# Kernel optimization log

Hardware: AMD Instinct MI355X
Metric: run time of the kernel (lower is better)

Reference implementation:

```python
import jax, jax.numpy as jnp
import numpy as np

B, H, W, DIM, WS, NH, HID = 16, 64, 64, 256, 8, 8, 1024
SHIFT = WS // 2
N = WS * WS  # tokens per window


def _rel_pos_index(ws):
    coords = np.stack(np.meshgrid(np.arange(ws), np.arange(ws), indexing='ij')).reshape(2, -1)
    rel = (coords[:, :, None] - coords[:, None, :]).transpose(1, 2, 0)  # [n,n,2]
    rel[..., 0] += ws - 1
    rel[..., 1] += ws - 1
    rel[..., 0] *= 2 * ws - 1
    return rel.sum(-1)  # [n,n] ints in [0, (2ws-1)^2)


def _attn_mask(h, w, ws, ss):
    img = np.zeros((h, w), np.float32)
    cnt = 0
    sl = (slice(0, -ws), slice(-ws, -ss), slice(-ss, None))
    for hs in sl:
        for wsl in sl:
            img[hs, wsl] = cnt
            cnt += 1
    mw = img.reshape(h // ws, ws, w // ws, ws).transpose(0, 2, 1, 3).reshape(-1, ws * ws)
    d = mw[:, None, :] - mw[:, :, None]  # unsqueeze(1) - unsqueeze(2)
    return np.where(d != 0, np.float32(-100.0), np.float32(0.0))  # [nW,n,n]


RPI = jnp.asarray(_rel_pos_index(WS).reshape(-1))          # [n*n] int
MASK = jnp.asarray(_attn_mask(H, W, WS, SHIFT))            # [nW,n,n]


def ln(x, g, b, eps):
    m = x.mean(-1, keepdims=True)
    v = x.var(-1, keepdims=True)
    return (x - m) / jnp.sqrt(v + eps) * g + b


def win_part(x, ws):
    b, h, w, c = x.shape
    x = x.reshape(b, h // ws, ws, w // ws, ws, c).transpose(0, 1, 3, 2, 4, 5)
    return x.reshape(-1, ws * ws, c)  # [b*nW, n, c]


def win_rev(win, ws, h, w):
    c = win.shape[-1]
    b = win.shape[0] // ((h // ws) * (w // ws))
    x = win.reshape(b, h // ws, w // ws, ws, ws, c).transpose(0, 1, 3, 2, 4, 5)
    return x.reshape(b, h, w, c)


def attention(xw, qkv_w, qkv_b, rpb, out_w, out_b, mask):
    Bw, n, c = xw.shape
    dh = c // NH
    scale = dh ** -0.5
    qkv = (xw @ qkv_w + qkv_b).reshape(Bw, n, 3, NH, dh).transpose(2, 0, 3, 1, 4)
    q, k, v = qkv[0], qkv[1], qkv[2]                       # [Bw,NH,n,dh]
    dots = jnp.einsum('bhid,bhjd->bhij', q, k) * scale
    bias = rpb[RPI].reshape(n, n, NH).transpose(2, 0, 1)   # [NH,n,n]
    attn = dots + bias[None]
    if mask is not None:
        nW = mask.shape[0]
        attn = attn.reshape(Bw // nW, nW, NH, n, n) + mask[None, :, None]
        attn = attn.reshape(Bw, NH, n, n)
    attn = jax.nn.softmax(attn, axis=-1)
    out = jnp.einsum('bhij,bhjd->bhid', attn, v)
    out = out.transpose(0, 2, 1, 3).reshape(Bw, n, c)
    return out @ out_w + out_b


def block(x, shifted, mask, n1g, n1b, qkv_w, qkv_b, rpb, out_w, out_b,
          n2g, n2b, lng, lnb, w1, b1, w2, b2):
    b, l, c = x.shape
    shortcut = x
    x = ln(x, n1g, n1b, 1e-5).reshape(b, H, W, c)
    if shifted:
        x = jnp.roll(x, (-SHIFT, -SHIFT), (1, 2))
    xw = win_part(x, WS)
    xw = attention(xw, qkv_w, qkv_b, rpb, out_w, out_b, mask)
    x = win_rev(xw, WS, H, W)
    if shifted:
        x = jnp.roll(x, (SHIFT, SHIFT), (1, 2))
    x = shortcut + x.reshape(b, l, c)
    # FeedForward contains its own LayerNorm(eps=1e-6) after norm2 (faithful to source)
    h = ln(x, n2g, n2b, 1e-5)
    h = ln(h, lng, lnb, 1e-6)
    h = jax.nn.gelu(h @ w1 + b1, approximate=False) @ w2 + b2
    return x + h


def forward(x, *p):
    x = block(x, False, None, *p[0:15])
    x = block(x, True, MASK, *p[15:30])
    return x


def setup_inputs() -> dict:
    key = jax.random.key(0)
    ks = iter(jax.random.split(key, 16))
    s = 0.02
    d = {'x': jax.random.normal(next(ks), (B, H * W, DIM), jnp.float32)}
    for i in (0, 1):
        p = f'b{i}_'
        d[p + 'n1g'] = jnp.ones((DIM,), jnp.float32)
        d[p + 'n1b'] = jnp.zeros((DIM,), jnp.float32)
        d[p + 'qkv_w'] = jax.random.normal(next(ks), (DIM, 3 * DIM), jnp.float32) * s
        d[p + 'qkv_b'] = jnp.zeros((3 * DIM,), jnp.float32)
        d[p + 'rpb'] = jax.random.normal(next(ks), ((2 * WS - 1) ** 2, NH), jnp.float32) * s
        d[p + 'out_w'] = jax.random.normal(next(ks), (DIM, DIM), jnp.float32) * s
        d[p + 'out_b'] = jnp.zeros((DIM,), jnp.float32)
        d[p + 'n2g'] = jnp.ones((DIM,), jnp.float32)
        d[p + 'n2b'] = jnp.zeros((DIM,), jnp.float32)
        d[p + 'lng'] = jnp.ones((DIM,), jnp.float32)
        d[p + 'lnb'] = jnp.zeros((DIM,), jnp.float32)
        d[p + 'w1'] = jax.random.normal(next(ks), (DIM, HID), jnp.float32) * s
        d[p + 'b1'] = jnp.zeros((HID,), jnp.float32)
        d[p + 'w2'] = jax.random.normal(next(ks), (HID, DIM), jnp.float32) * s
        d[p + 'b2'] = jnp.zeros((DIM,), jnp.float32)
    return d


def reference(x,
              b0_n1g, b0_n1b, b0_qkv_w, b0_qkv_b, b0_rpb, b0_out_w, b0_out_b,
              b0_n2g, b0_n2b, b0_lng, b0_lnb, b0_w1, b0_b1, b0_w2, b0_b2,
              b1_n1g, b1_n1b, b1_qkv_w, b1_qkv_b, b1_rpb, b1_out_w, b1_out_b,
              b1_n2g, b1_n2b, b1_lng, b1_lnb, b1_w1, b1_b1, b1_w2, b1_b2):
    return forward(x,
                   b0_n1g, b0_n1b, b0_qkv_w, b0_qkv_b, b0_rpb, b0_out_w, b0_out_b,
                   b0_n2g, b0_n2b, b0_lng, b0_lnb, b0_w1, b0_b1, b0_w2, b0_b2,
                   b1_n1g, b1_n1b, b1_qkv_w, b1_qkv_b, b1_rpb, b1_out_w, b1_out_b,
                   b1_n2g, b1_n2b, b1_lng, b1_lnb, b1_w1, b1_b1, b1_w2, b1_b2)
```

## Files before the change

### kernel.cpp

```cpp
#include <hip/hip_runtime.h>

typedef unsigned short u16;
typedef __attribute__((ext_vector_type(8))) short bf16x8;
typedef __attribute__((ext_vector_type(8))) unsigned short u16x8;
typedef __attribute__((ext_vector_type(4))) unsigned short u16x4;
typedef __attribute__((ext_vector_type(4))) float f32x4;

__device__ inline float b2f(u16 u) {
    union { unsigned u32; float f; } x; x.u32 = ((unsigned)u) << 16; return x.f;
}
__device__ inline u16 f2b(float f) {
    union { float f; unsigned u; } x; x.f = f;
    unsigned r = x.u + 0x7fffu + ((x.u >> 16) & 1u);
    return (u16)(r >> 16);
}

#define GLOAD_LDS16(g, l) \
    __builtin_amdgcn_global_load_lds((const __attribute__((address_space(1))) void*)(const void*)(g), \
                                     (__attribute__((address_space(3))) void*)(void*)(l), 16, 0, 0)

__global__ __launch_bounds__(256)
void ln_win_kernel(const float* __restrict__ x, const float* __restrict__ g,
                   const float* __restrict__ b, u16* __restrict__ xw, int shift)
{
    int wid = blockIdx.x * 4 + (threadIdx.x >> 6);
    int lane = threadIdx.x & 63;
    int win = wid >> 6, tok = wid & 63;
    int bb = win >> 6, wib = win & 63;
    int h = (((wib >> 3) << 3) + (tok >> 3) + shift) & 63;
    int w = (((wib & 7) << 3) + (tok & 7) + shift) & 63;
    size_t src = ((size_t)bb * 4096 + h * 64 + w) * 256;
    float4 v = ((const float4*)(x + src))[lane];
    float s = v.x + v.y + v.z + v.w;
    float s2 = v.x*v.x + v.y*v.y + v.z*v.z + v.w*v.w;
    for (int k = 32; k > 0; k >>= 1) { s += __shfl_xor(s, k); s2 += __shfl_xor(s2, k); }
    float mean = s * (1.f/256.f);
    float var  = s2 * (1.f/256.f) - mean*mean;
    float rs = rsqrtf(var + 1e-5f);
    int c = lane * 4;
    u16x4 o;
    o[0] = f2b((v.x - mean) * rs * g[c+0] + b[c+0]);
    o[1] = f2b((v.y - mean) * rs * g[c+1] + b[c+1]);
    o[2] = f2b((v.z - mean) * rs * g[c+2] + b[c+2]);
    o[3] = f2b((v.w - mean) * rs * g[c+3] + b[c+3]);
    *(u16x4*)(xw + (size_t)wid * 256 + c) = o;
}

__global__ __launch_bounds__(256)
void ln2_kernel(const float* __restrict__ xin,
                const float* __restrict__ g1, const float* __restrict__ b1,
                const float* __restrict__ g2, const float* __restrict__ b2,
                u16* __restrict__ out)
{
    int wid = blockIdx.x * 4 + (threadIdx.x >> 6);
    int lane = threadIdx.x & 63;
    float4 v = ((const float4*)(xin + (size_t)wid * 256))[lane];
    float s = v.x + v.y + v.z + v.w;
    float s2 = v.x*v.x + v.y*v.y + v.z*v.z + v.w*v.w;
    for (int k = 32; k > 0; k >>= 1) { s += __shfl_xor(s, k); s2 += __shfl_xor(s2, k); }
    float mean = s * (1.f/256.f);
    float var  = s2 * (1.f/256.f) - mean*mean;
    float rs = rsqrtf(var + 1e-5f);
    int c = lane * 4;
    float y0 = (v.x - mean) * rs * g1[c+0] + b1[c+0];
    float y1 = (v.y - mean) * rs * g1[c+1] + b1[c+1];
    float y2 = (v.z - mean) * rs * g1[c+2] + b1[c+2];
    float y3 = (v.w - mean) * rs * g1[c+3] + b1[c+3];
    float t = y0 + y1 + y2 + y3;
    float t2 = y0*y0 + y1*y1 + y2*y2 + y3*y3;
    for (int k = 32; k > 0; k >>= 1) { t += __shfl_xor(t, k); t2 += __shfl_xor(t2, k); }
    float m2 = t * (1.f/256.f);
    float v2 = t2 * (1.f/256.f) - m2*m2;
    float rs2 = rsqrtf(v2 + 1e-6f);
    u16x4 o;
    o[0] = f2b((y0 - m2) * rs2 * g2[c+0] + b2[c+0]);
    o[1] = f2b((y1 - m2) * rs2 * g2[c+1] + b2[c+1]);
    o[2] = f2b((y2 - m2) * rs2 * g2[c+2] + b2[c+2]);
    o[3] = f2b((y3 - m2) * rs2 * g2[c+3] + b2[c+3]);
    *(u16x4*)(out + (size_t)wid * 256 + c) = o;
}

__global__ __launch_bounds__(256)
void transpose_w(const float* __restrict__ W, u16* __restrict__ Wt, int K, int N)
{
    __shared__ float t[32][33];
    int nb = blockIdx.x * 32, kb = blockIdx.y * 32;
    int tx = threadIdx.x & 31, ty = threadIdx.x >> 5;
    #pragma unroll
    for (int r = 0; r < 32; r += 8)
        t[ty + r][tx] = W[(size_t)(kb + ty + r) * N + nb + tx];
    __syncthreads();
    #pragma unroll
    for (int r = 0; r < 32; r += 8)
        Wt[(size_t)(nb + ty + r) * K + kb + tx] = f2b(t[tx][ty + r]);
}

__global__ __launch_bounds__(256)
void build_bias(const float* __restrict__ rpb, float* __restrict__ bmT)
{
    int idx = blockIdx.x * 256 + threadIdx.x;
    int q = idx & 63, k = (idx >> 6) & 63, h = (idx >> 12) & 7, cls = idx >> 15;
    int qh = q >> 3, qw = q & 7, kh = k >> 3, kw = k & 7;
    float v = rpb[((qh - kh + 7) * 15 + (qw - kw + 7)) * 8 + h];
    int ch = cls >> 1, cw = cls & 1;
    int rq = (ch ? (qh < 4 ? 1 : 2) : 0) * 3 + (cw ? (qw < 4 ? 1 : 2) : 0);
    int rk = (ch ? (kh < 4 ? 1 : 2) : 0) * 3 + (cw ? (kw < 4 ? 1 : 2) : 0);
    if (rq != rk) v -= 100.f;
    bmT[idx] = v * 1.4426950408889634f;
}

template<int EPI>
__global__ __launch_bounds__(256)
void gemm_bf16(const u16* __restrict__ A, const u16* __restrict__ Bt,
               const float* __restrict__ bias, void* __restrict__ out,
               const float* __restrict__ resid, int M, int N, int K, int shift)
{
    __shared__ u16 As[128 * 32];
    __shared__ u16 Bs[128 * 32];
    const int tid = threadIdx.x;
    const int lane = tid & 63, wv = tid >> 6;
    const int bm = blockIdx.y, bn = blockIdx.x;
    const int wr = wv >> 1, wc = wv & 1;
    f32x4 acc[4][4] = {};
    const int arow = wv * 16 + (lane >> 2);
    const int acol = (lane & 3) * 8;
    const u16* gA = A + (size_t)(bm * 128 + arow) * K + acol;
    const u16* gB = Bt + (size_t)(bn * 128 + arow) * K + acol;
    const int nk = K >> 5;
    for (int kt = 0; kt < nk; ++kt) {
        __syncthreads();
        GLOAD_LDS16(gA,          As + wv * 512);
        GLOAD_LDS16(gA + 64 * K, As + 2048 + wv * 512);
        GLOAD_LDS16(gB,          Bs + wv * 512);
        GLOAD_LDS16(gB + 64 * K, Bs + 2048 + wv * 512);
        gA += 32; gB += 32;
        __syncthreads();
        const int g = lane >> 4, r = lane & 15;
        bf16x8 af[4], bf[4];
        #pragma unroll
        for (int i = 0; i < 4; ++i)
            af[i] = *(const bf16x8*)(As + (wr * 64 + i * 16 + r) * 32 + g * 8);
        #pragma unroll
        for (int i = 0; i < 4; ++i)
            bf[i] = *(const bf16x8*)(Bs + (wc * 64 + i * 16 + r) * 32 + g * 8);
        #pragma unroll
        for (int i = 0; i < 4; ++i)
            #pragma unroll
            for (int j = 0; j < 4; ++j)
                acc[i][j] = __builtin_amdgcn_mfma_f32_16x16x32_bf16(af[i], bf[j], acc[i][j], 0, 0, 0);
    }
    const int r4 = (lane >> 4) * 4;
    const int cn = lane & 15;
    #pragma unroll
    for (int i = 0; i < 4; ++i) {
        #pragma unroll
        for (int rr = 0; rr < 4; ++rr) {
            int row = bm * 128 + wr * 64 + i * 16 + r4 + rr;
            size_t orow;
            if (EPI == 2) {
                int win = row >> 6, tok = row & 63;
                int bb = win >> 6, wib = win & 63;
                int h = (((wib >> 3) << 3) + (tok >> 3) + shift) & 63;
                int w = (((wib & 7) << 3) + (tok & 7) + shift) & 63;
                orow = (size_t)bb * 4096 + h * 64 + w;
            } else {
                orow = (size_t)row;
            }
            #pragma unroll
            for (int j = 0; j < 4; ++j) {
                int col = bn * 128 + wc * 64 + j * 16 + cn;
                float v = acc[i][j][rr] + bias[col];
                if (EPI == 0) {
                    ((u16*)out)[(size_t)row * N + col] = f2b(v);
                } else if (EPI == 1) {
                    float ge = 0.5f * v * (1.f + erff(v * 0.70710678118654752f));
                    ((u16*)out)[(size_t)row * N + col] = f2b(ge);
                } else {
                    ((float*)out)[orow * N + col] = resid[orow * N + col] + v;
                }
            }
        }
    }
}

template<int SHIFTED>
__global__ __launch_bounds__(256)
void attn_mfma(const u16* __restrict__ qkv, const float* __restrict__ bmT,
               u16* __restrict__ out)
{
    __shared__ u16 pbuf[4][64 * 72];
    __shared__ u16 vbuf[4][32 * 72];
    const int tid = threadIdx.x, lane = tid & 63, wv = tid >> 6;
    const int g = lane >> 4, r = lane & 15;
    const int win = blockIdx.x;
    u16* P  = pbuf[wv];
    u16* Vt = vbuf[wv];
    const u16* base = qkv + (size_t)win * 64 * 768;
    int cls = 0;
    if (SHIFTED) {
        int wib = win & 63;
        cls = (((wib >> 3) == 7) ? 2 : 0) + (((wib & 7) == 7) ? 1 : 0);
    }
    const float sc = 0.17677669529663687f * 1.4426950408889634f;

    for (int hh = 0; hh < 2; ++hh) {
        const int h = wv * 2 + hh;
        const float* bmh = bmT + ((size_t)cls * 8 + h) * 4096;
        bf16x8 kf[4], qf[4];
        #pragma unroll
        for (int i = 0; i < 4; ++i) {
            kf[i] = *(const bf16x8*)(base + (size_t)(i * 16 + r) * 768 + 256 + h * 32 + g * 8);
            qf[i] = *(const bf16x8*)(base + (size_t)(i * 16 + r) * 768 +       h * 32 + g * 8);
        }
        #pragma unroll
        for (int d0 = 0; d0 < 32; d0 += 8) {
            u16x8 vv = *(const u16x8*)(base + (size_t)lane * 768 + 512 + h * 32 + d0);
            #pragma unroll
            for (int e = 0; e < 8; ++e) Vt[(d0 + e) * 72 + lane] = vv[e];
        }
        f32x4 acc[4][4] = {};
        #pragma unroll
        for (int i = 0; i < 4; ++i)
            #pragma unroll
            for (int j = 0; j < 4; ++j)
                acc[i][j] = __builtin_amdgcn_mfma_f32_16x16x32_bf16(kf[i], qf[j], acc[i][j], 0, 0, 0);
        #pragma unroll
        for (int i = 0; i < 4; ++i) {
            const int kb = (i * 16 + g * 4) * 64;
            #pragma unroll
            for (int j = 0; j < 4; ++j) {
                const int qq = j * 16 + r;
                #pragma unroll
                for (int rr = 0; rr < 4; ++rr)
                    acc[i][j][rr] = acc[i][j][rr] * sc + bmh[kb + rr * 64 + qq];
            }
        }
        float inv_[4];
        #pragma unroll
        for (int j = 0; j < 4; ++j) {
            float m = acc[0][j][0];
            #pragma unroll
            for (int i = 0; i < 4; ++i)
                #pragma unroll
                for (int rr = 0; rr < 4; ++rr) m = fmaxf(m, acc[i][j][rr]);
            m = fmaxf(m, __shfl_xor(m, 16));
            m = fmaxf(m, __shfl_xor(m, 32));
            float s = 0.f;
            #pragma unroll
            for (int i = 0; i < 4; ++i)
                #pragma unroll
                for (int rr = 0; rr < 4; ++rr) {
                    float p = exp2f(acc[i][j][rr] - m);
                    acc[i][j][rr] = p; s += p;
                }
            s += __shfl_xor(s, 16);
            s += __shfl_xor(s, 32);
            inv_[j] = 1.f / s;
        }
        #pragma unroll
        for (int j = 0; j < 4; ++j) {
            const float iv = inv_[j];
            #pragma unroll
            for (int i = 0; i < 4; ++i) {
                u16x4 w;
                #pragma unroll
                for (int rr = 0; rr < 4; ++rr) w[rr] = f2b(acc[i][j][rr] * iv);
                *(u16x4*)(P + (j * 16 + r) * 72 + i * 16 + g * 4) = w;
            }
        }
        f32x4 o[4][2] = {};
        #pragma unroll
        for (int ks = 0; ks < 2; ++ks) {
            bf16x8 pa[4], vb[2];
            #pragma unroll
            for (int i = 0; i < 4; ++i)
                pa[i] = *(const bf16x8*)(P + (i * 16 + r) * 72 + ks * 32 + g * 8);
            #pragma unroll
            for (int j = 0; j < 2; ++j)
                vb[j] = *(const bf16x8*)(Vt + (j * 16 + r) * 72 + ks * 32 + g * 8);
            #pragma unroll
            for (int i = 0; i < 4; ++i)
                #pragma unroll
                for (int j = 0; j < 2; ++j)
                    o[i][j] = __builtin_amdgcn_mfma_f32_16x16x32_bf16(pa[i], vb[j], o[i][j], 0, 0, 0);
        }
        u16* op = out + (size_t)win * 64 * 256 + h * 32;
        #pragma unroll
        for (int i = 0; i < 4; ++i)
            #pragma unroll
            for (int j = 0; j < 2; ++j)
                #pragma unroll
                for (int rr = 0; rr < 4; ++rr)
                    op[(size_t)(i * 16 + g * 4 + rr) * 256 + j * 16 + r] = f2b(o[i][j][rr]);
    }
}

extern "C" void kernel_launch(void* const* d_in, const int* in_sizes, int n_in,
                              void* d_out, int out_size, void* d_ws, size_t ws_size,
                              hipStream_t stream)
{
    (void)in_sizes; (void)n_in; (void)out_size; (void)ws_size;
    const float* x = (const float*)d_in[0];
    char* ws = (char*)d_ws;
    size_t off = 0;
    auto alloc = [&](size_t bytes) { void* p = ws + off; off += (bytes + 255) & ~(size_t)255; return p; };

    u16 *wtq[2], *wto[2], *wt1[2], *wt2[2];
    float* bmT[2];
    for (int i = 0; i < 2; ++i) {
        wtq[i] = (u16*)alloc((size_t)768 * 256 * 2);
        wto[i] = (u16*)alloc((size_t)256 * 256 * 2);
        wt1[i] = (u16*)alloc((size_t)1024 * 256 * 2);
        wt2[i] = (u16*)alloc((size_t)256 * 1024 * 2);
        bmT[i] = (float*)alloc((size_t)4 * 8 * 64 * 64 * 4);
    }
    u16*  xw  = (u16*)alloc((size_t)65536 * 256 * 2);
    u16*  big = (u16*)alloc((size_t)65536 * 1024 * 2);
    float* x1 = (float*)alloc((size_t)65536 * 256 * 4);
    float* outp = (float*)d_out;

    for (int blk = 0; blk < 2; ++blk) {
        const float* const* P = (const float* const*)(d_in + 1 + blk * 15);
        transpose_w<<<dim3(768 / 32, 256 / 32), 256, 0, stream>>>(P[2], wtq[blk], 256, 768);
        transpose_w<<<dim3(256 / 32, 256 / 32), 256, 0, stream>>>(P[5], wto[blk], 256, 256);
        transpose_w<<<dim3(1024 / 32, 256 / 32), 256, 0, stream>>>(P[11], wt1[blk], 256, 1024);
        transpose_w<<<dim3(256 / 32, 1024 / 32), 256, 0, stream>>>(P[13], wt2[blk], 1024, 256);
        build_bias<<<512, 256, 0, stream>>>(P[4], bmT[blk]);
    }

    for (int blk = 0; blk < 2; ++blk) {
        const float* const* P = (const float* const*)(d_in + 1 + blk * 15);
        const int sh = blk ? 4 : 0;
        const float* xin = blk ? outp : x;

        ln_win_kernel<<<16384, 256, 0, stream>>>(xin, P[0], P[1], xw, sh);
        gemm_bf16<0><<<dim3(6, 512), 256, 0, stream>>>(xw, wtq[blk], P[3], big, nullptr, 65536, 768, 256, 0);
        if (blk) attn_mfma<1><<<1024, 256, 0, stream>>>(big, bmT[blk], xw);
        else     attn_mfma<0><<<1024, 256, 0, stream>>>(big, bmT[blk], xw);
        gemm_bf16<2><<<dim3(2, 512), 256, 0, stream>>>(xw, wto[blk], P[6], x1, xin, 65536, 256, 256, sh);
        ln2_kernel<<<16384, 256, 0, stream>>>(x1, P[7], P[8], P[9], P[10], xw);
        gemm_bf16<1><<<dim3(8, 512), 256, 0, stream>>>(xw, wt1[blk], P[12], big, nullptr, 65536, 1024, 256, 0);
        gemm_bf16<3><<<dim3(2, 512), 256, 0, stream>>>(big, wt2[blk], P[14], outp, x1, 65536, 256, 1024, 0);
    }
}
```

Measured before the change: 748.8 us.

## Fuse MLP GEMMs with GELU through LDS and vectorize GEMM epilogues

Replaces the separate fc1+GELU and fc2+residual GEMMs with one fused kernel that keeps the 1024-wide hidden activations for a 64-row tile in shared memory, avoiding writing and re-reading the large hidden tensor. GEMM and attention MFMA operands are swapped so each lane holds contiguous columns, enabling vectorized bias/residual loads and stores. The GEMM grid is remapped so consecutive tiles land on the same XCD. The fused kernel loads operands straight from global memory without LDS staging, relying on caches for weight reuse.

```diff
diff --git a/kernel.cpp b/kernel.cpp
--- a/kernel.cpp
+++ b/kernel.cpp
@@ -119,7 +119,12 @@
     __shared__ u16 Bs[128 * 32];
     const int tid = threadIdx.x;
     const int lane = tid & 63, wv = tid >> 6;
-    const int bm = blockIdx.y, bn = blockIdx.x;
+    const int nwg = gridDim.x * gridDim.y;
+    const int lid = blockIdx.y * gridDim.x + blockIdx.x;
+    const int qq = nwg >> 3, r8 = nwg & 7;
+    const int xcd = lid & 7, pos = lid >> 3;
+    const int nid = (xcd < r8 ? xcd * (qq + 1) : r8 * (qq + 1) + (xcd - r8) * qq) + pos;
+    const int bm = nid / gridDim.x, bn = nid % gridDim.x;
     const int wr = wv >> 1, wc = wv & 1;
     f32x4 acc[4][4] = {};
     const int arow = wv * 16 + (lane >> 2);
@@ -127,6 +132,7 @@
     const u16* gA = A + (size_t)(bm * 128 + arow) * K + acol;
     const u16* gB = Bt + (size_t)(bn * 128 + arow) * K + acol;
     const int nk = K >> 5;
+    const int g = lane >> 4, r = lane & 15;
     for (int kt = 0; kt < nk; ++kt) {
         __syncthreads();
         GLOAD_LDS16(gA,          As + wv * 512);
@@ -135,7 +141,6 @@
         GLOAD_LDS16(gB + 64 * K, Bs + 2048 + wv * 512);
         gA += 32; gB += 32;
         __syncthreads();
-        const int g = lane >> 4, r = lane & 15;
         bf16x8 af[4], bf[4];
         #pragma unroll
         for (int i = 0; i < 4; ++i)
@@ -144,41 +149,125 @@
         for (int i = 0; i < 4; ++i)
             bf[i] = *(const bf16x8*)(Bs + (wc * 64 + i * 16 + r) * 32 + g * 8);
         #pragma unroll
-        for (int i = 0; i < 4; ++i)
-            #pragma unroll
-            for (int j = 0; j < 4; ++j)
-                acc[i][j] = __builtin_amdgcn_mfma_f32_16x16x32_bf16(af[i], bf[j], acc[i][j], 0, 0, 0);
-    }
-    const int r4 = (lane >> 4) * 4;
-    const int cn = lane & 15;
+        for (int j = 0; j < 4; ++j)
+            #pragma unroll
+            for (int i = 0; i < 4; ++i)
+                acc[j][i] = __builtin_amdgcn_mfma_f32_16x16x32_bf16(bf[j], af[i], acc[j][i], 0, 0, 0);
+    }
     #pragma unroll
     for (int i = 0; i < 4; ++i) {
-        #pragma unroll
-        for (int rr = 0; rr < 4; ++rr) {
-            int row = bm * 128 + wr * 64 + i * 16 + r4 + rr;
-            size_t orow;
-            if (EPI == 2) {
-                int win = row >> 6, tok = row & 63;
-                int bb = win >> 6, wib = win & 63;
-                int h = (((wib >> 3) << 3) + (tok >> 3) + shift) & 63;
-                int w = (((wib & 7) << 3) + (tok & 7) + shift) & 63;
-                orow = (size_t)bb * 4096 + h * 64 + w;
+        const int row = bm * 128 + wr * 64 + i * 16 + r;
+        size_t orow;
+        if (EPI == 2) {
+            int win = row >> 6, tok = row & 63;
+            int bb = win >> 6, wib = win & 63;
+            int h = (((wib >> 3) << 3) + (tok >> 3) + shift) & 63;
+            int w = (((wib & 7) << 3) + (tok & 7) + shift) & 63;
+            orow = (size_t)bb * 4096 + h * 64 + w;
+        } else {
+            orow = (size_t)row;
+        }
+        #pragma unroll
+        for (int j = 0; j < 4; ++j) {
+            const int colb = bn * 128 + wc * 64 + j * 16 + g * 4;
+            const float4 bv = *(const float4*)(bias + colb);
+            if (EPI == 0) {
+                u16x4 o;
+                o[0] = f2b(acc[j][i][0] + bv.x);
+                o[1] = f2b(acc[j][i][1] + bv.y);
+                o[2] = f2b(acc[j][i][2] + bv.z);
+                o[3] = f2b(acc[j][i][3] + bv.w);
+                *(u16x4*)((u16*)out + (size_t)row * N + colb) = o;
             } else {
-                orow = (size_t)row;
+                const float4 rv = *(const float4*)(resid + orow * N + colb);
+                float4 o;
+                o.x = rv.x + acc[j][i][0] + bv.x;
+                o.y = rv.y + acc[j][i][1] + bv.y;
+                o.z = rv.z + acc[j][i][2] + bv.z;
+                o.w = rv.w + acc[j][i][3] + bv.w;
+                *(float4*)((float*)out + orow * N + colb) = o;
             }
-            #pragma unroll
-            for (int j = 0; j < 4; ++j) {
-                int col = bn * 128 + wc * 64 + j * 16 + cn;
-                float v = acc[i][j][rr] + bias[col];
-                if (EPI == 0) {
-                    ((u16*)out)[(size_t)row * N + col] = f2b(v);
-                } else if (EPI == 1) {
-                    float ge = 0.5f * v * (1.f + erff(v * 0.70710678118654752f));
-                    ((u16*)out)[(size_t)row * N + col] = f2b(ge);
-                } else {
-                    ((float*)out)[orow * N + col] = resid[orow * N + col] + v;
+        }
+    }
+}
+
+__global__ __launch_bounds__(256, 2)
+void fused_mlp(const u16* __restrict__ A, const u16* __restrict__ W1t,
+               const float* __restrict__ b1, const u16* __restrict__ W2t,
+               const float* __restrict__ b2, const float* __restrict__ x1,
+               float* __restrict__ out)
+{
+    __shared__ u16 Hs[64][264];
+    const int tid = threadIdx.x, lane = tid & 63, wv = tid >> 6;
+    const int g = lane >> 4, r = lane & 15;
+    const size_t row0 = (size_t)blockIdx.x * 64;
+    f32x4 p2[4][4] = {};
+    for (int q = 0; q < 4; ++q) {
+        f32x4 p1[4][4] = {};
+        const u16* w1p = W1t + ((size_t)q * 256 + wv * 64) * 256;
+        #pragma unroll
+        for (int ks = 0; ks < 8; ++ks) {
+            bf16x8 af[4], wb[4];
+            #pragma unroll
+            for (int i = 0; i < 4; ++i)
+                af[i] = *(const bf16x8*)(A + (row0 + i * 16 + r) * 256 + ks * 32 + g * 8);
+            #pragma unroll
+            for (int j = 0; j < 4; ++j)
+                wb[j] = *(const bf16x8*)(w1p + (size_t)(j * 16 + r) * 256 + ks * 32 + g * 8);
+            #pragma unroll
+            for (int j = 0; j < 4; ++j)
+                #pragma unroll
+                for (int i = 0; i < 4; ++i)
+                    p1[j][i] = __builtin_amdgcn_mfma_f32_16x16x32_bf16(wb[j], af[i], p1[j][i], 0, 0, 0);
+        }
+        __syncthreads();
+        #pragma unroll
+        for (int j = 0; j < 4; ++j) {
+            const int cq = wv * 64 + j * 16 + g * 4;
+            const float4 bv = *(const float4*)(b1 + q * 256 + cq);
+            #pragma unroll
+            for (int i = 0; i < 4; ++i) {
+                u16x4 hw;
+                #pragma unroll
+                for (int rr = 0; rr < 4; ++rr) {
+                    float v = p1[j][i][rr] + ((const float*)&bv)[rr];
+                    hw[rr] = f2b(0.5f * v * (1.f + erff(v * 0.70710678118654752f)));
                 }
+                *(u16x4*)(&Hs[i * 16 + r][cq]) = hw;
             }
+        }
+        __syncthreads();
+        const u16* w2p = W2t + (size_t)(wv * 64) * 1024 + q * 256;
+        #pragma unroll
+        for (int ks = 0; ks < 8; ++ks) {
+            bf16x8 hf[4], w2[4];
+            #pragma unroll
+            for (int i = 0; i < 4; ++i)
+                hf[i] = *(const bf16x8*)(&Hs[i * 16 + r][ks * 32 + g * 8]);
+            #pragma unroll
+            for (int j = 0; j < 4; ++j)
+                w2[j] = *(const bf16x8*)(w2p + (size_t)(j * 16 + r) * 1024 + ks * 32 + g * 8);
+            #pragma unroll
+            for (int j = 0; j < 4; ++j)
+                #pragma unroll
+                for (int i = 0; i < 4; ++i)
+                    p2[j][i] = __builtin_amdgcn_mfma_f32_16x16x32_bf16(w2[j], hf[i], p2[j][i], 0, 0, 0);
+        }
+    }
+    #pragma unroll
+    for (int j = 0; j < 4; ++j) {
+        const int col = wv * 64 + j * 16 + g * 4;
+        const float4 bv = *(const float4*)(b2 + col);
+        #pragma unroll
+        for (int i = 0; i < 4; ++i) {
+            const size_t row = row0 + i * 16 + r;
+            const float4 rv = *(const float4*)(x1 + row * 256 + col);
+            float4 o;
+            o.x = rv.x + p2[j][i][0] + bv.x;
+            o.y = rv.y + p2[j][i][1] + bv.y;
+            o.z = rv.z + p2[j][i][2] + bv.z;
+            o.w = rv.w + p2[j][i][3] + bv.w;
+            *(float4*)(out + row * 256 + col) = o;
         }
     }
 }
@@ -268,7 +357,7 @@
                 *(u16x4*)(P + (j * 16 + r) * 72 + i * 16 + g * 4) = w;
             }
         }
-        f32x4 o[4][2] = {};
+        f32x4 o[2][4] = {};
         #pragma unroll
         for (int ks = 0; ks < 2; ++ks) {
             bf16x8 pa[4], vb[2];
@@ -279,19 +368,23 @@
             for (int j = 0; j < 2; ++j)
                 vb[j] = *(const bf16x8*)(Vt + (j * 16 + r) * 72 + ks * 32 + g * 8);
             #pragma unroll
-            for (int i = 0; i < 4; ++i)
-                #pragma unroll
-                for (int j = 0; j < 2; ++j)
-                    o[i][j] = __builtin_amdgcn_mfma_f32_16x16x32_bf16(pa[i], vb[j], o[i][j], 0, 0, 0);
+            for (int j = 0; j < 2; ++j)
+                #pragma unroll
+                for (int i = 0; i < 4; ++i)
+                    o[j][i] = __builtin_amdgcn_mfma_f32_16x16x32_bf16(vb[j], pa[i], o[j][i], 0, 0, 0);
         }
         u16* op = out + (size_t)win * 64 * 256 + h * 32;
         #pragma unroll
-        for (int i = 0; i < 4; ++i)
-            #pragma unroll
-            for (int j = 0; j < 2; ++j)
-                #pragma unroll
-                for (int rr = 0; rr < 4; ++rr)
-                    op[(size_t)(i * 16 + g * 4 + rr) * 256 + j * 16 + r] = f2b(o[i][j][rr]);
+        for (int i = 0; i < 4; ++i) {
+            const int qrow = i * 16 + r;
+            #pragma unroll
+            for (int j = 0; j < 2; ++j) {
+                u16x4 w;
+                #pragma unroll
+                for (int rr = 0; rr < 4; ++rr) w[rr] = f2b(o[j][i][rr]);
+                *(u16x4*)(op + (size_t)qrow * 256 + j * 16 + g * 4) = w;
+            }
+        }
     }
 }
 
@@ -315,7 +408,7 @@
         bmT[i] = (float*)alloc((size_t)4 * 8 * 64 * 64 * 4);
     }
     u16*  xw  = (u16*)alloc((size_t)65536 * 256 * 2);
-    u16*  big = (u16*)alloc((size_t)65536 * 1024 * 2);
+    u16*  big = (u16*)alloc((size_t)65536 * 768 * 2);
     float* x1 = (float*)alloc((size_t)65536 * 256 * 4);
     float* outp = (float*)d_out;
 
@@ -339,7 +432,6 @@
         else     attn_mfma<0><<<1024, 256, 0, stream>>>(big, bmT[blk], xw);
         gemm_bf16<2><<<dim3(2, 512), 256, 0, stream>>>(xw, wto[blk], P[6], x1, xin, 65536, 256, 256, sh);
         ln2_kernel<<<16384, 256, 0, stream>>>(x1, P[7], P[8], P[9], P[10], xw);
-        gemm_bf16<1><<<dim3(8, 512), 256, 0, stream>>>(xw, wt1[blk], P[12], big, nullptr, 65536, 1024, 256, 0);
-        gemm_bf16<3><<<dim3(2, 512), 256, 0, stream>>>(big, wt2[blk], P[14], outp, x1, 65536, 256, 1024, 0);
-    }
-}
+        fused_mlp<<<1024, 256, 0, stream>>>(xw, wt1[blk], P[12], wt2[blk], P[14], x1, outp);
+    }
+}
```

Result: slower. 919.1 us (+22.7%).

## Pipeline GEMM with 4-stage LDS ring, swizzle, XCD remap, vectorized epilogues

Applied to the files above, without the earlier changes.

Replaces the single-buffered GEMM with a 4-slot LDS ring that prefetches two k-tiles ahead, using explicit vmcnt waits and one barrier per iteration. It XOR-swizzles LDS columns to avoid bank conflicts and remaps workgroups to XCDs for cache locality. Operands are swapped in the MFMA so each lane holds four consecutive columns, which allows vectorized bias, residual and output stores; the attention PV output uses the same trick. GELU switches to a polynomial erf approximation, which adds small numeric error.

```diff
diff --git a/kernel.cpp b/kernel.cpp
--- a/kernel.cpp
+++ b/kernel.cpp
@@ -15,9 +15,21 @@
     return (u16)(r >> 16);
 }
 
+__device__ inline float fast_gelu(float v) {
+    float x = fabsf(v) * 0.70710678118654752f;
+    float t = __builtin_amdgcn_rcpf(1.0f + 0.3275911f * x);
+    float e = __expf(-x * x);
+    float poly = ((((1.061405429f * t - 1.453152027f) * t + 1.421413741f) * t
+                   - 0.284496736f) * t + 0.254829592f) * t;
+    float erfv = 1.0f - poly * e;
+    float w = copysignf(erfv, v);
+    return 0.5f * v * (1.0f + w);
+}
+
 #define GLOAD_LDS16(g, l) \
     __builtin_amdgcn_global_load_lds((const __attribute__((address_space(1))) void*)(const void*)(g), \
                                      (__attribute__((address_space(3))) void*)(void*)(l), 16, 0, 0)
+#define FENCE() asm volatile("" ::: "memory")
 
 __global__ __launch_bounds__(256)
 void ln_win_kernel(const float* __restrict__ x, const float* __restrict__ g,
@@ -111,73 +123,110 @@
 
 template<int EPI>
 __global__ __launch_bounds__(256)
-void gemm_bf16(const u16* __restrict__ A, const u16* __restrict__ Bt,
-               const float* __restrict__ bias, void* __restrict__ out,
-               const float* __restrict__ resid, int M, int N, int K, int shift)
-{
-    __shared__ u16 As[128 * 32];
-    __shared__ u16 Bs[128 * 32];
-    const int tid = threadIdx.x;
-    const int lane = tid & 63, wv = tid >> 6;
-    const int bm = blockIdx.y, bn = blockIdx.x;
+void gemm_k4(const u16* __restrict__ A, const u16* __restrict__ Bt,
+             const float* __restrict__ bias, void* __restrict__ out,
+             const float* __restrict__ resid, int M, int N, int K, int shift)
+{
+    __shared__ u16 As[4][128][32];
+    __shared__ u16 Bs[4][128][32];
+    const int tid = threadIdx.x, lane = tid & 63, wv = tid >> 6;
+    const int g = lane >> 4, r = lane & 15;
     const int wr = wv >> 1, wc = wv & 1;
+    const int nwg = gridDim.x * gridDim.y;
+    const int lid = blockIdx.y * gridDim.x + blockIdx.x;
+    const int qq = nwg >> 3, r8 = nwg & 7;
+    const int xcd = lid & 7, pos = lid >> 3;
+    const int nid = (xcd < r8 ? xcd * (qq + 1) : r8 * (qq + 1) + (xcd - r8) * qq) + pos;
+    const int bm = nid / gridDim.x, bn = nid % gridDim.x;
+
     f32x4 acc[4][4] = {};
     const int arow = wv * 16 + (lane >> 2);
-    const int acol = (lane & 3) * 8;
-    const u16* gA = A + (size_t)(bm * 128 + arow) * K + acol;
-    const u16* gB = Bt + (size_t)(bn * 128 + arow) * K + acol;
+    const int scol = (((lane & 3) ^ ((lane >> 2) & 3) ^ ((lane >> 4) & 1)) * 8);
+    const u16* gA = A + (size_t)(bm * 128 + arow) * K + scol;
+    const u16* gB = Bt + (size_t)(bn * 128 + arow) * K + scol;
     const int nk = K >> 5;
+    const int rc = (g ^ (r & 3) ^ ((r >> 2) & 1)) * 8;
+
+#define STAGE(t) do { \
+        u16* a_ = &As[(t) & 3][0][0]; u16* b_ = &Bs[(t) & 3][0][0]; \
+        GLOAD_LDS16(gA + (size_t)(t) * 32,                    a_ + wv * 512); \
+        GLOAD_LDS16(gA + (size_t)(t) * 32 + (size_t)64 * K,   a_ + 2048 + wv * 512); \
+        GLOAD_LDS16(gB + (size_t)(t) * 32,                    b_ + wv * 512); \
+        GLOAD_LDS16(gB + (size_t)(t) * 32 + (size_t)64 * K,   b_ + 2048 + wv * 512); \
+    } while (0)
+
+    STAGE(0);
+    STAGE(1);
     for (int kt = 0; kt < nk; ++kt) {
-        __syncthreads();
-        GLOAD_LDS16(gA,          As + wv * 512);
-        GLOAD_LDS16(gA + 64 * K, As + 2048 + wv * 512);
-        GLOAD_LDS16(gB,          Bs + wv * 512);
-        GLOAD_LDS16(gB + 64 * K, Bs + 2048 + wv * 512);
-        gA += 32; gB += 32;
-        __syncthreads();
-        const int g = lane >> 4, r = lane & 15;
+        const int cur = kt & 3;
+        if (kt + 2 < nk) {
+            STAGE(kt + 2);
+            asm volatile("s_waitcnt vmcnt(8)" ::: "memory");
+        } else if (kt + 1 < nk) {
+            asm volatile("s_waitcnt vmcnt(4)" ::: "memory");
+        } else {
+            asm volatile("s_waitcnt vmcnt(0)" ::: "memory");
+        }
+        __builtin_amdgcn_s_barrier();
+        FENCE();
         bf16x8 af[4], bf[4];
         #pragma unroll
         for (int i = 0; i < 4; ++i)
-            af[i] = *(const bf16x8*)(As + (wr * 64 + i * 16 + r) * 32 + g * 8);
-        #pragma unroll
-        for (int i = 0; i < 4; ++i)
-            bf[i] = *(const bf16x8*)(Bs + (wc * 64 + i * 16 + r) * 32 + g * 8);
-        #pragma unroll
-        for (int i = 0; i < 4; ++i)
-            #pragma unroll
-            for (int j = 0; j < 4; ++j)
-                acc[i][j] = __builtin_amdgcn_mfma_f32_16x16x32_bf16(af[i], bf[j], acc[i][j], 0, 0, 0);
-    }
-    const int r4 = (lane >> 4) * 4;
-    const int cn = lane & 15;
+            af[i] = *(const bf16x8*)(&As[cur][wr * 64 + i * 16 + r][rc]);
+        #pragma unroll
+        for (int j = 0; j < 4; ++j)
+            bf[j] = *(const bf16x8*)(&Bs[cur][wc * 64 + j * 16 + r][rc]);
+        __builtin_amdgcn_s_setprio(1);
+        #pragma unroll
+        for (int j = 0; j < 4; ++j)
+            #pragma unroll
+            for (int i = 0; i < 4; ++i)
+                acc[j][i] = __builtin_amdgcn_mfma_f32_16x16x32_bf16(bf[j], af[i], acc[j][i], 0, 0, 0);
+        __builtin_amdgcn_s_setprio(0);
+        asm volatile("s_waitcnt lgkmcnt(0)" ::: "memory");
+        __builtin_amdgcn_sched_barrier(0);
+    }
+#undef STAGE
+
     #pragma unroll
     for (int i = 0; i < 4; ++i) {
-        #pragma unroll
-        for (int rr = 0; rr < 4; ++rr) {
-            int row = bm * 128 + wr * 64 + i * 16 + r4 + rr;
-            size_t orow;
-            if (EPI == 2) {
-                int win = row >> 6, tok = row & 63;
-                int bb = win >> 6, wib = win & 63;
-                int h = (((wib >> 3) << 3) + (tok >> 3) + shift) & 63;
-                int w = (((wib & 7) << 3) + (tok & 7) + shift) & 63;
-                orow = (size_t)bb * 4096 + h * 64 + w;
+        const int row = bm * 128 + wr * 64 + i * 16 + r;
+        size_t orow;
+        if (EPI == 2) {
+            int win = row >> 6, tok = row & 63;
+            int bb = win >> 6, wib = win & 63;
+            int h = (((wib >> 3) << 3) + (tok >> 3) + shift) & 63;
+            int w = (((wib & 7) << 3) + (tok & 7) + shift) & 63;
+            orow = (size_t)bb * 4096 + h * 64 + w;
+        } else {
+            orow = (size_t)row;
+        }
+        #pragma unroll
+        for (int j = 0; j < 4; ++j) {
+            const int colb = bn * 128 + wc * 64 + j * 16 + g * 4;
+            const float4 bv = *(const float4*)(bias + colb);
+            if (EPI == 0) {
+                u16x4 o;
+                o[0] = f2b(acc[j][i][0] + bv.x);
+                o[1] = f2b(acc[j][i][1] + bv.y);
+                o[2] = f2b(acc[j][i][2] + bv.z);
+                o[3] = f2b(acc[j][i][3] + bv.w);
+                *(u16x4*)((u16*)out + (size_t)row * N + colb) = o;
+            } else if (EPI == 1) {
+                u16x4 o;
+                o[0] = f2b(fast_gelu(acc[j][i][0] + bv.x));
+                o[1] = f2b(fast_gelu(acc[j][i][1] + bv.y));
+                o[2] = f2b(fast_gelu(acc[j][i][2] + bv.z));
+                o[3] = f2b(fast_gelu(acc[j][i][3] + bv.w));
+                *(u16x4*)((u16*)out + (size_t)row * N + colb) = o;
             } else {
-                orow = (size_t)row;
-            }
-            #pragma unroll
-            for (int j = 0; j < 4; ++j) {
-                int col = bn * 128 + wc * 64 + j * 16 + cn;
-                float v = acc[i][j][rr] + bias[col];
-                if (EPI == 0) {
-                    ((u16*)out)[(size_t)row * N + col] = f2b(v);
-                } else if (EPI == 1) {
-                    float ge = 0.5f * v * (1.f + erff(v * 0.70710678118654752f));
-                    ((u16*)out)[(size_t)row * N + col] = f2b(ge);
-                } else {
-                    ((float*)out)[orow * N + col] = resid[orow * N + col] + v;
-                }
+                const float4 rv = *(const float4*)(resid + orow * N + colb);
+                float4 o;
+                o.x = rv.x + acc[j][i][0] + bv.x;
+                o.y = rv.y + acc[j][i][1] + bv.y;
+                o.z = rv.z + acc[j][i][2] + bv.z;
+                o.w = rv.w + acc[j][i][3] + bv.w;
+                *(float4*)((float*)out + orow * N + colb) = o;
             }
         }
     }
@@ -268,7 +317,7 @@
                 *(u16x4*)(P + (j * 16 + r) * 72 + i * 16 + g * 4) = w;
             }
         }
-        f32x4 o[4][2] = {};
+        f32x4 o[2][4] = {};
         #pragma unroll
         for (int ks = 0; ks < 2; ++ks) {
             bf16x8 pa[4], vb[2];
@@ -279,19 +328,23 @@
             for (int j = 0; j < 2; ++j)
                 vb[j] = *(const bf16x8*)(Vt + (j * 16 + r) * 72 + ks * 32 + g * 8);
             #pragma unroll
-            for (int i = 0; i < 4; ++i)
-                #pragma unroll
-                for (int j = 0; j < 2; ++j)
-                    o[i][j] = __builtin_amdgcn_mfma_f32_16x16x32_bf16(pa[i], vb[j], o[i][j], 0, 0, 0);
+            for (int j = 0; j < 2; ++j)
+                #pragma unroll
+                for (int i = 0; i < 4; ++i)
+                    o[j][i] = __builtin_amdgcn_mfma_f32_16x16x32_bf16(vb[j], pa[i], o[j][i], 0, 0, 0);
         }
         u16* op = out + (size_t)win * 64 * 256 + h * 32;
         #pragma unroll
-        for (int i = 0; i < 4; ++i)
-            #pragma unroll
-            for (int j = 0; j < 2; ++j)
-                #pragma unroll
-                for (int rr = 0; rr < 4; ++rr)
-                    op[(size_t)(i * 16 + g * 4 + rr) * 256 + j * 16 + r] = f2b(o[i][j][rr]);
+        for (int i = 0; i < 4; ++i) {
+            const int qrow = i * 16 + r;
+            #pragma unroll
+            for (int j = 0; j < 2; ++j) {
+                u16x4 w;
+                #pragma unroll
+                for (int rr = 0; rr < 4; ++rr) w[rr] = f2b(o[j][i][rr]);
+                *(u16x4*)(op + (size_t)qrow * 256 + j * 16 + g * 4) = w;
+            }
+        }
     }
 }
 
@@ -334,12 +387,12 @@
         const float* xin = blk ? outp : x;
 
         ln_win_kernel<<<16384, 256, 0, stream>>>(xin, P[0], P[1], xw, sh);
-        gemm_bf16<0><<<dim3(6, 512), 256, 0, stream>>>(xw, wtq[blk], P[3], big, nullptr, 65536, 768, 256, 0);
+        gemm_k4<0><<<dim3(6, 512), 256, 0, stream>>>(xw, wtq[blk], P[3], big, nullptr, 65536, 768, 256, 0);
         if (blk) attn_mfma<1><<<1024, 256, 0, stream>>>(big, bmT[blk], xw);
         else     attn_mfma<0><<<1024, 256, 0, stream>>>(big, bmT[blk], xw);
-        gemm_bf16<2><<<dim3(2, 512), 256, 0, stream>>>(xw, wto[blk], P[6], x1, xin, 65536, 256, 256, sh);
+        gemm_k4<2><<<dim3(2, 512), 256, 0, stream>>>(xw, wto[blk], P[6], x1, xin, 65536, 256, 256, sh);
         ln2_kernel<<<16384, 256, 0, stream>>>(x1, P[7], P[8], P[9], P[10], xw);
-        gemm_bf16<1><<<dim3(8, 512), 256, 0, stream>>>(xw, wt1[blk], P[12], big, nullptr, 65536, 1024, 256, 0);
-        gemm_bf16<3><<<dim3(2, 512), 256, 0, stream>>>(big, wt2[blk], P[14], outp, x1, 65536, 256, 1024, 0);
-    }
-}
+        gemm_k4<1><<<dim3(8, 512), 256, 0, stream>>>(xw, wt1[blk], P[12], big, nullptr, 65536, 1024, 256, 0);
+        gemm_k4<3><<<dim3(2, 512), 256, 0, stream>>>(big, wt2[blk], P[14], outp, x1, 65536, 256, 1024, 0);
+    }
+}
```

After: 723.1 us. 1.04x faster.
